# Performance work log

Measured on AMD Instinct MI355X. Metric: run time of the kernel, lower is better.

The kernel has to match this reference:

```python
import jax, jax.numpy as jnp
import numpy as np

THRESHOLD_PERCENTILE = 0.8  # init arg
B, H, W, C, N = 4, 256, 256, 128, 32


def _label_components(mask):
    """8-connected components via iterative min-label propagation.
    Background pixels get sentinel label BIG (== scipy label 0)."""
    h, w = mask.shape
    big = h * w
    init = jnp.where(mask, jnp.arange(big, dtype=jnp.int32).reshape(h, w), jnp.int32(big))

    def propagate(lbl):
        p = jnp.pad(lbl, 1, constant_values=big)
        # min over the 3x3 (8-connected incl. self) neighborhood
        nb = jnp.min(jnp.stack([p[di:di + h, dj:dj + w]
                                for di in range(3) for dj in range(3)]), axis=0)
        return jnp.where(mask, nb, jnp.int32(big))

    def cond(state):
        return ~state[1]

    def body(state):
        lbl, _ = state
        new = propagate(lbl)
        return new, jnp.all(new == lbl)

    lbl, _ = jax.lax.while_loop(cond, body, (init, jnp.array(False)))
    return lbl, jnp.int32(big)


def _merged_pairs_one(feat, centers):
    """feat: [H,W,C] float; centers: [N,2] int32. Returns merged-pair count."""
    h, w, c = feat.shape
    gt = feat[centers[:, 0], centers[:, 1]]                    # [N,C]
    flat = feat.reshape(-1, c)                                 # [HW,C]
    # euclidean cdist via norms (torch.cdist p=2)
    d2 = (jnp.sum(flat * flat, axis=1)[:, None]
          + jnp.sum(gt * gt, axis=1)[None, :]
          - 2.0 * flat @ gt.T)                                 # [HW,N]
    dists = jnp.sqrt(jnp.maximum(d2, 0.0))
    contrast = dists.min(axis=1).reshape(h, w)                 # [H,W]
    thr = jnp.percentile(contrast, THRESHOLD_PERCENTILE * 100.0)
    mask = contrast >= thr
    lbl, big = _label_components(mask)
    ids = lbl[centers[:, 0], centers[:, 1]]                    # [N]
    valid = ids != big                                         # scipy label > 0
    eq = (ids[:, None] == ids[None, :]) & valid[:, None]
    n = centers.shape[0]
    triu = jnp.triu(jnp.ones((n, n), dtype=bool), 1)           # i < j pairs
    return jnp.sum(eq & triu)


def setup_inputs() -> dict:
    key = jax.random.key(0)
    k1, k2 = jax.random.split(key)
    features = jax.random.normal(k1, (B, H, W, C), dtype=jnp.float32)
    gt_centers = jax.random.randint(k2, (B, N, 2), 0, H, dtype=jnp.int64)
    return {"features": features, "gt_centers": gt_centers}


def reference(features, gt_centers):
    centers = gt_centers.astype(jnp.int32)
    merged = jax.vmap(_merged_pairs_one)(features, centers)    # [B]
    n = centers.shape[1]
    total_pairs = features.shape[0] * (n * (n - 1) // 2)
    merge_rate = merged.sum().astype(jnp.float32) / jnp.float32(total_pairs)
    return merge_rate
```

## Files before the change

kernel.cpp:

```cpp
#include <hip/hip_runtime.h>
#include <stdint.h>

#define BB 4
#define HH 256
#define WW 256
#define CC 128
#define NN 32
#define NPIX (HH*WW)
#define RANK 52428u
#define TOTAL_PAIRS 1984.0f
#define CAND_MAX 8192u

#define OFF_KEYS 0
#define OFF_P    (BB*NPIX*4)
#define OFF_HIST (OFF_P + BB*NPIX*4)
#define OFF_THR  (OFF_HIST + BB*1024*4)
#define ZERO_BYTES (BB*1024*4)

typedef __attribute__((ext_vector_type(8))) short short8;
typedef __attribute__((ext_vector_type(4))) float f32x4;

__device__ __forceinline__ void split3(float f, short &hi, short &mid, short &lo) {
    uint32_t u  = __float_as_uint(f);
    uint32_t hb = u & 0xffff0000u;
    hi = (short)(hb >> 16);
    float r1 = f - __uint_as_float(hb);
    uint32_t mb = __float_as_uint(r1) & 0xffff0000u;
    mid = (short)(mb >> 16);
    float r2 = r1 - __uint_as_float(mb);
    lo = (short)(__float_as_uint(r2) >> 16);
}

__device__ __forceinline__ uint32_t qbin_of(uint32_t keybits) {
    float f = __uint_as_float(keybits);
    return (uint32_t)fminf(f * 128.0f, 65535.0f);
}

__global__ __launch_bounds__(256) void k_d2mfma(const float* __restrict__ feat,
        const int* __restrict__ centers, uint32_t* __restrict__ keys,
        uint32_t* __restrict__ hist) {
    __shared__ short gB[12288];
    __shared__ float gpart[32][8];
    __shared__ float gnormL[32];
    __shared__ uint32_t lhist[1024];
    int b = blockIdx.y;
    int tid = threadIdx.x;

    #pragma unroll
    for (int j = 0; j < 4; j++) lhist[tid + j*256] = 0u;

    {
        int n = tid & 31, j0 = tid >> 5;
        int cy = centers[(b*NN + n)*2 + 0];
        int cx = centers[(b*NN + n)*2 + 1];
        const float* gp = feat + ((size_t)(b << 16) + cy*WW + cx)*CC + j0*16;
        int tt = n >> 4, lane16 = n & 15, kk = j0 >> 1, qbase = (j0 & 1)*2;
        float ss = 0.f;
        #pragma unroll
        for (int hh = 0; hh < 2; hh++) {
            short8 vhi, vmid, vlo;
            #pragma unroll
            for (int u = 0; u < 8; u++) {
                float f = gp[hh*8 + u];
                ss = fmaf(f, f, ss);
                short a, bm, c; split3(f, a, bm, c);
                vhi[u] = a; vmid[u] = bm; vlo[u] = c;
            }
            int lane = (qbase + hh)*16 + lane16;
            int off = (tt*4 + kk)*512 + lane*8;
            *(short8*)&gB[off]        = vhi;
            *(short8*)&gB[off + 4096] = vmid;
            *(short8*)&gB[off + 8192] = vlo;
        }
        gpart[n][j0] = ss;
    }
    __syncthreads();
    if (tid < 32) {
        float s = 0.f;
        #pragma unroll
        for (int j = 0; j < 8; j++) s += gpart[tid][j];
        gnormL[tid] = s;
    }
    __syncthreads();

    int wv = tid >> 6, L = tid & 63;
    int m = L & 15, q = L >> 4;
    float gn0 = gnormL[m];
    float gn1 = gnormL[16 + m];

    for (int it = 0; it < 4; it++) {
        int p0 = blockIdx.x*256 + (wv*4 + it)*16;
        const float* fp = feat + ((size_t)(b << 16) + p0 + m)*CC + q*8;

        f32x4 acc[2] = {{0.f,0.f,0.f,0.f},{0.f,0.f,0.f,0.f}};
        float fn = 0.f;

        #pragma unroll
        for (int kk = 0; kk < 4; kk++) {
            float4 fa = *(const float4*)(fp + kk*32);
            float4 fb = *(const float4*)(fp + kk*32 + 4);
            float fs[8] = {fa.x,fa.y,fa.z,fa.w,fb.x,fb.y,fb.z,fb.w};
            short8 ahi, amid, alo;
            #pragma unroll
            for (int j = 0; j < 8; j++) {
                float f = fs[j];
                fn = fmaf(f, f, fn);
                short hh, md, lw; split3(f, hh, md, lw);
                ahi[j] = hh; amid[j] = md; alo[j] = lw;
            }
            #pragma unroll
            for (int t = 0; t < 2; t++) {
                int off = (t*4 + kk)*512 + L*8;
                short8 bhi = *(const short8*)&gB[off];
                short8 bmd = *(const short8*)&gB[off + 4096];
                short8 blo = *(const short8*)&gB[off + 8192];
                acc[t] = __builtin_amdgcn_mfma_f32_16x16x32_bf16(ahi,  bhi, acc[t], 0,0,0);
                acc[t] = __builtin_amdgcn_mfma_f32_16x16x32_bf16(ahi,  bmd, acc[t], 0,0,0);
                acc[t] = __builtin_amdgcn_mfma_f32_16x16x32_bf16(amid, bhi, acc[t], 0,0,0);
                acc[t] = __builtin_amdgcn_mfma_f32_16x16x32_bf16(ahi,  blo, acc[t], 0,0,0);
                acc[t] = __builtin_amdgcn_mfma_f32_16x16x32_bf16(amid, bmd, acc[t], 0,0,0);
                acc[t] = __builtin_amdgcn_mfma_f32_16x16x32_bf16(alo,  bhi, acc[t], 0,0,0);
            }
        }

        fn += __shfl_xor(fn, 16);
        fn += __shfl_xor(fn, 32);

        float vmin[4];
        #pragma unroll
        for (int r = 0; r < 4; r++) {
            float fnr = __shfl(fn, q*4 + r);
            float d0 = fnr + gn0 - 2.f*acc[0][r];
            float d1 = fnr + gn1 - 2.f*acc[1][r];
            float v = fminf(d0, d1);
            v = fminf(v, __shfl_xor(v, 1));
            v = fminf(v, __shfl_xor(v, 2));
            v = fminf(v, __shfl_xor(v, 4));
            v = fminf(v, __shfl_xor(v, 8));
            vmin[r] = v;
        }
        if (m < 4) {
            float v = (m==0) ? vmin[0] : (m==1) ? vmin[1] : (m==2) ? vmin[2] : vmin[3];
            if (!(v > 0.f)) v = 0.f;
            uint32_t kb = __float_as_uint(v);
            keys[(size_t)(b << 16) + p0 + q*4 + m] = kb;
            atomicAdd(&lhist[qbin_of(kb) >> 6], 1u);
        }
    }

    __syncthreads();
    #pragma unroll
    for (int j = 0; j < 4; j++) {
        int bin = tid + j*256;
        uint32_t hv = lhist[bin];
        if (hv) atomicAdd(&hist[(b << 10) + bin], hv);
    }
}

__global__ __launch_bounds__(1024) void k_selthr(const uint32_t* __restrict__ keys,
        const uint32_t* __restrict__ hist, uint32_t* __restrict__ thr_sm) {
    int b = blockIdx.x, t = threadIdx.x;
    __shared__ uint32_t wsum[16];
    __shared__ uint32_t sT1, sR1, sT, sR2, scnt, scnt2;
    __shared__ uint32_t fh[64];
    __shared__ uint32_t cand[CAND_MAX];
    __shared__ uint32_t cand2[2048];

    if (t < 64) fh[t] = 0;
    if (t == 0) { scnt = 0; scnt2 = 0; }

    int lane = t & 63, w = t >> 6;
    uint32_t s = hist[(b << 10) + t];
    uint32_t inc = s;
    #pragma unroll
    for (int off = 1; off < 64; off <<= 1) {
        uint32_t nb = __shfl_up((int)inc, off);
        if (lane >= off) inc += nb;
    }
    if (lane == 63) wsum[w] = inc;
    __syncthreads();
    if (t < 16) {
        uint32_t v = wsum[t];
        #pragma unroll
        for (int off = 1; off < 16; off <<= 1) {
            uint32_t nb = __shfl_up((int)v, off);
            if (t >= off) v += nb;
        }
        wsum[t] = v;
    }
    __syncthreads();
    uint32_t pre = ((w == 0) ? 0u : wsum[w-1]) + inc - s;
    if (pre <= RANK && RANK < pre + s) { sT1 = (uint32_t)t; sR1 = RANK - pre; }
    __syncthreads();
    uint32_t T1 = sT1, r1 = sR1;

    const uint4* kb = (const uint4*)(keys + ((size_t)b << 16));
    for (int i = t; i < NPIX/4; i += 1024) {
        uint4 k = kb[i];
        uint32_t q;
        #define PROC_KEY(X) { q = qbin_of(X); if ((q >> 6) == T1) { \
            atomicAdd(&fh[q & 63u], 1u); \
            uint32_t p = atomicAdd(&scnt, 1u); \
            if (p < CAND_MAX) cand[p] = (X); } }
        PROC_KEY(k.x) PROC_KEY(k.y) PROC_KEY(k.z) PROC_KEY(k.w)
        #undef PROC_KEY
    }
    __syncthreads();

    if (t < 64) {
        uint32_t s2 = fh[t];
        uint32_t inc2 = s2;
        #pragma unroll
        for (int off = 1; off < 64; off <<= 1) {
            uint32_t nb = __shfl_up((int)inc2, off);
            if (t >= off) inc2 += nb;
        }
        uint32_t pre2 = inc2 - s2;
        if (pre2 <= r1 && r1 < pre2 + s2) { sT = (T1 << 6) | (uint32_t)t; sR2 = r1 - pre2; }
    }
    __syncthreads();
    uint32_t T = sT, r2 = sR2;
    uint32_t K = scnt; if (K > CAND_MAX) K = CAND_MAX;

    for (uint32_t i = t; i < K; i += 1024) {
        uint32_t v = cand[i];
        if (qbin_of(v) == T) { uint32_t p = atomicAdd(&scnt2, 1u); if (p < 2048u) cand2[p] = v; }
    }
    __syncthreads();
    uint32_t K2 = scnt2; if (K2 > 2048u) K2 = 2048u;

    for (uint32_t i = t; i < K2; i += 1024) {
        uint32_t v = cand2[i];
        uint32_t less = 0, eq = 0;
        for (uint32_t j = 0; j < K2; j++) { uint32_t x = cand2[j]; less += (x < v); eq += (x == v); }
        if (less <= r2 && r2 < less + eq) thr_sm[b] = v;
    }
}

__global__ __launch_bounds__(256) void k_initrun(const uint32_t* __restrict__ keys,
        const uint32_t* __restrict__ thr_sm, int* __restrict__ P) {
    int b = blockIdx.y;
    int row = blockIdx.x, x = threadIdx.x;
    int p = row*256 + x;
    uint32_t thr = thr_sm[b];
    bool msk = keys[(b << 16) + p] >= thr;

    __shared__ int wmax[4];
    int lane = x & 63, w = x >> 6;
    int v = msk ? -1 : x;
    #pragma unroll
    for (int off = 1; off < 64; off <<= 1) {
        int nb = __shfl_up(v, off);
        if (lane >= off) v = max(v, nb);
    }
    if (lane == 63) wmax[w] = v;
    __syncthreads();
    int acc = v;
    for (int i = 0; i < w; i++) acc = max(acc, wmax[i]);
    P[(b << 16) + p] = msk ? (row*256 + acc + 1) : -1;
}

__device__ __forceinline__ int uf_find(int* P, int x) {
    while (true) {
        int p = P[x];
        if (p == x) return x;
        int gp = P[p];
        if (gp != p) P[x] = gp;
        x = gp;
    }
}
__device__ __forceinline__ void uf_unite(int* P, int a, int b) {
    while (true) {
        a = uf_find(P, a);
        b = uf_find(P, b);
        if (a == b) return;
        if (a > b) { int t = a; a = b; b = t; }
        int old = atomicCAS(&P[b], b, a);
        if (old == b) return;
        b = old;
    }
}
__global__ __launch_bounds__(256) void k_union(int* __restrict__ Pg) {
    int b = blockIdx.y;
    int p = blockIdx.x*256 + threadIdx.x;
    int* P = Pg + (b << 16);
    if (P[p] == -1) return;
    int y = p >> 8, x = p & 255;
    if (y == 0) return;
    bool ul = (x > 0)   && P[p-WW-1] != -1;
    bool uu =              P[p-WW]   != -1;
    bool ur = (x < 255) && P[p-WW+1] != -1;
    if (ul)        uf_unite(P, p, p-WW-1);
    if (uu && !ul) uf_unite(P, p, p-WW);
    if (ur && !uu) uf_unite(P, p, p-WW+1);
}

__global__ void k_pairs_fin(const int* __restrict__ centers, int* __restrict__ Pg,
                            float* __restrict__ out) {
    __shared__ int ids[BB*NN];
    __shared__ int total;
    int t = threadIdx.x;
    if (t == 0) total = 0;
    __syncthreads();
    if (t < BB*NN) {
        int b = t >> 5;
        int cy = centers[t*2 + 0];
        int cx = centers[t*2 + 1];
        int p = cy*WW + cx;
        const int* P = Pg + (b << 16);
        int id = P[p];
        if (id != -1) {
            int x = p;
            while (true) { int q = P[x]; if (q == x) break; x = q; }
            id = x;
        }
        ids[t] = id;
    }
    __syncthreads();
    int cnt = 0;
    if (t < BB*NN) {
        int b = t >> 5, n = t & 31;
        int id = ids[t];
        if (id != -1) for (int j = n+1; j < NN; j++) cnt += (ids[b*NN + j] == id);
    }
    if (cnt) atomicAdd(&total, cnt);
    __syncthreads();
    if (t == 0) out[0] = (float)total / TOTAL_PAIRS;
}

extern "C" void kernel_launch(void* const* d_in, const int* in_sizes, int n_in,
                              void* d_out, int out_size, void* d_ws, size_t ws_size,
                              hipStream_t stream) {
    const float* feat  = (const float*)d_in[0];
    const int* centers = (const int*)d_in[1];
    float* out         = (float*)d_out;
    char* ws           = (char*)d_ws;

    uint32_t* keys = (uint32_t*)(ws + OFF_KEYS);
    int*      Pg   = (int*)(ws + OFF_P);
    uint32_t* hist = (uint32_t*)(ws + OFF_HIST);
    uint32_t* thr  = (uint32_t*)(ws + OFF_THR);

    hipMemsetAsync(ws + OFF_HIST, 0, ZERO_BYTES, stream);

    dim3 gridPix(NPIX/256, BB);
    k_d2mfma    <<<gridPix, 256, 0, stream>>>(feat, centers, keys, hist);
    k_selthr    <<<BB, 1024, 0, stream>>>(keys, hist, thr);
    k_initrun   <<<gridPix, 256, 0, stream>>>(keys, thr, Pg);
    k_union     <<<gridPix, 256, 0, stream>>>(Pg);
    k_pairs_fin <<<1, 256, 0, stream>>>(centers, Pg, out);
}
```

Before: 232.8 us.

## Fuse CCL init, union and pair counting into one kernel with last-block finish

Merges the row-run init, union-find and pair-count kernels into a single kernel. Each block recomputes row-start labels for its own row and the row above in shared memory, unites only the run representatives, and the last block to finish (tracked by an atomic counter) counts the merged pairs. Parent storage becomes a zero-means-root encoding, so the memset initialises the union-find array instead of a separate write pass. This removes two kernel launches and a full label-array write pass, at the cost of a larger memset, duplicated scan work per block and a threadfence-based completion protocol.

```diff
diff --git a/kernel.cpp b/kernel.cpp
--- a/kernel.cpp
+++ b/kernel.cpp
@@ -11,11 +11,12 @@
 #define TOTAL_PAIRS 1984.0f
 #define CAND_MAX 8192u
 
-#define OFF_KEYS 0
-#define OFF_P    (BB*NPIX*4)
-#define OFF_HIST (OFF_P + BB*NPIX*4)
-#define OFF_THR  (OFF_HIST + BB*1024*4)
-#define ZERO_BYTES (BB*1024*4)
+#define OFF_HIST 0
+#define OFF_DONE (BB*1024*4)
+#define OFF_P    (OFF_DONE + 64)
+#define ZERO_BYTES (OFF_P + BB*NPIX*4)
+#define OFF_THR  ZERO_BYTES
+#define OFF_KEYS (OFF_THR + 64)
 
 typedef __attribute__((ext_vector_type(8))) short short8;
 typedef __attribute__((ext_vector_type(4))) float f32x4;
@@ -237,36 +238,15 @@
     }
 }
 
-__global__ __launch_bounds__(256) void k_initrun(const uint32_t* __restrict__ keys,
-        const uint32_t* __restrict__ thr_sm, int* __restrict__ P) {
-    int b = blockIdx.y;
-    int row = blockIdx.x, x = threadIdx.x;
-    int p = row*256 + x;
-    uint32_t thr = thr_sm[b];
-    bool msk = keys[(b << 16) + p] >= thr;
-
-    __shared__ int wmax[4];
-    int lane = x & 63, w = x >> 6;
-    int v = msk ? -1 : x;
-    #pragma unroll
-    for (int off = 1; off < 64; off <<= 1) {
-        int nb = __shfl_up(v, off);
-        if (lane >= off) v = max(v, nb);
-    }
-    if (lane == 63) wmax[w] = v;
-    __syncthreads();
-    int acc = v;
-    for (int i = 0; i < w; i++) acc = max(acc, wmax[i]);
-    P[(b << 16) + p] = msk ? (row*256 + acc + 1) : -1;
-}
-
 __device__ __forceinline__ int uf_find(int* P, int x) {
     while (true) {
-        int p = P[x];
-        if (p == x) return x;
-        int gp = P[p];
-        if (gp != p) P[x] = gp;
-        x = gp;
+        int v = P[x];
+        if (v == 0) return x;
+        int p = v - 1;
+        int gv = P[p];
+        if (gv == 0) return p;
+        P[x] = gv;
+        x = gv - 1;
     }
 }
 __device__ __forceinline__ void uf_unite(int* P, int a, int b) {
@@ -275,57 +255,103 @@
         b = uf_find(P, b);
         if (a == b) return;
         if (a > b) { int t = a; a = b; b = t; }
-        int old = atomicCAS(&P[b], b, a);
-        if (old == b) return;
-        b = old;
-    }
-}
-__global__ __launch_bounds__(256) void k_union(int* __restrict__ Pg) {
-    int b = blockIdx.y;
-    int p = blockIdx.x*256 + threadIdx.x;
+        int old = atomicCAS(&P[b], 0, a + 1);
+        if (old == 0) return;
+        b = old - 1;
+    }
+}
+
+__global__ __launch_bounds__(256) void k_ccl(const uint32_t* __restrict__ keys,
+        const uint32_t* __restrict__ thr_sm, const int* __restrict__ centers,
+        int* __restrict__ Pg, uint32_t* __restrict__ done, float* __restrict__ out) {
+    int bid = blockIdx.x;
+    int b = bid >> 8, rr = bid & 255;
+    int x = threadIdx.x;
+    __shared__ int up_rs[256];
+    __shared__ int swtmp[4];
+    __shared__ int ids[BB*NN];
+    __shared__ int stotal;
+    __shared__ bool isLast;
+
+    uint32_t thrv = thr_sm[b];
     int* P = Pg + (b << 16);
-    if (P[p] == -1) return;
-    int y = p >> 8, x = p & 255;
-    if (y == 0) return;
-    bool ul = (x > 0)   && P[p-WW-1] != -1;
-    bool uu =              P[p-WW]   != -1;
-    bool ur = (x < 255) && P[p-WW+1] != -1;
-    if (ul)        uf_unite(P, p, p-WW-1);
-    if (uu && !ul) uf_unite(P, p, p-WW);
-    if (ur && !uu) uf_unite(P, p, p-WW+1);
-}
-
-__global__ void k_pairs_fin(const int* __restrict__ centers, int* __restrict__ Pg,
-                            float* __restrict__ out) {
-    __shared__ int ids[BB*NN];
-    __shared__ int total;
-    int t = threadIdx.x;
-    if (t == 0) total = 0;
-    __syncthreads();
-    if (t < BB*NN) {
-        int b = t >> 5;
-        int cy = centers[t*2 + 0];
-        int cx = centers[t*2 + 1];
-        int p = cy*WW + cx;
-        const int* P = Pg + (b << 16);
-        int id = P[p];
-        if (id != -1) {
-            int x = p;
-            while (true) { int q = P[x]; if (q == x) break; x = q; }
-            id = x;
-        }
-        ids[t] = id;
+    int p = (rr << 8) + x;
+    bool msk = keys[((size_t)b << 16) + p] >= thrv;
+    int lane = x & 63, w = x >> 6;
+
+    int v = msk ? -1 : x;
+    #pragma unroll
+    for (int off = 1; off < 64; off <<= 1) {
+        int nb = __shfl_up(v, off);
+        if (lane >= off) v = max(v, nb);
+    }
+    if (lane == 63) swtmp[w] = v;
+    __syncthreads();
+    int acc = v;
+    for (int i = 0; i < w; i++) acc = max(acc, swtmp[i]);
+    int rs = (rr << 8) + acc + 1;
+    __syncthreads();
+
+    if (rr > 0) {
+        bool msku = keys[((size_t)b << 16) + p - WW] >= thrv;
+        int vu = msku ? -1 : x;
+        #pragma unroll
+        for (int off = 1; off < 64; off <<= 1) {
+            int nb = __shfl_up(vu, off);
+            if (lane >= off) vu = max(vu, nb);
+        }
+        if (lane == 63) swtmp[w] = vu;
+        __syncthreads();
+        int accu = vu;
+        for (int i = 0; i < w; i++) accu = max(accu, swtmp[i]);
+        up_rs[x] = msku ? (((rr - 1) << 8) + accu + 1) : -1;
+    }
+
+    if (msk && rs != p) P[p] = rs + 1;
+    __syncthreads();
+
+    if (rr > 0 && msk) {
+        bool ul = (x > 0)   && up_rs[x-1] >= 0;
+        bool uu =              up_rs[x]   >= 0;
+        bool ur = (x < 255) && up_rs[x+1] >= 0;
+        if (ul)        uf_unite(P, rs, up_rs[x-1]);
+        if (uu && !ul) uf_unite(P, rs, up_rs[x]);
+        if (ur && !uu) uf_unite(P, rs, up_rs[x+1]);
+    }
+
+    __threadfence();
+    __syncthreads();
+    if (x == 0) { uint32_t d = atomicAdd(done, 1u); isLast = (d == 1023u); }
+    __syncthreads();
+    if (!isLast) return;
+    __threadfence();
+
+    if (x == 0) stotal = 0;
+    __syncthreads();
+    if (x < BB*NN) {
+        int bb = x >> 5;
+        int cy = centers[x*2 + 0];
+        int cx = centers[x*2 + 1];
+        int pp = cy*WW + cx;
+        const int* Pb = Pg + (bb << 16);
+        int id = -1;
+        if (keys[((size_t)bb << 16) + pp] >= thr_sm[bb]) {
+            int xx = pp;
+            while (true) { int vv = Pb[xx]; if (vv == 0) break; xx = vv - 1; }
+            id = xx;
+        }
+        ids[x] = id;
     }
     __syncthreads();
     int cnt = 0;
-    if (t < BB*NN) {
-        int b = t >> 5, n = t & 31;
-        int id = ids[t];
-        if (id != -1) for (int j = n+1; j < NN; j++) cnt += (ids[b*NN + j] == id);
-    }
-    if (cnt) atomicAdd(&total, cnt);
-    __syncthreads();
-    if (t == 0) out[0] = (float)total / TOTAL_PAIRS;
+    if (x < BB*NN) {
+        int bb = x >> 5, n = x & 31;
+        int id = ids[x];
+        if (id != -1) for (int j = n + 1; j < NN; j++) cnt += (ids[bb*NN + j] == id);
+    }
+    if (cnt) atomicAdd(&stotal, cnt);
+    __syncthreads();
+    if (x == 0) out[0] = (float)stotal / TOTAL_PAIRS;
 }
 
 extern "C" void kernel_launch(void* const* d_in, const int* in_sizes, int n_in,
@@ -336,17 +362,16 @@
     float* out         = (float*)d_out;
     char* ws           = (char*)d_ws;
 
+    uint32_t* hist = (uint32_t*)(ws + OFF_HIST);
+    uint32_t* done = (uint32_t*)(ws + OFF_DONE);
+    int*      Pg   = (int*)(ws + OFF_P);
+    uint32_t* thr  = (uint32_t*)(ws + OFF_THR);
     uint32_t* keys = (uint32_t*)(ws + OFF_KEYS);
-    int*      Pg   = (int*)(ws + OFF_P);
-    uint32_t* hist = (uint32_t*)(ws + OFF_HIST);
-    uint32_t* thr  = (uint32_t*)(ws + OFF_THR);
-
-    hipMemsetAsync(ws + OFF_HIST, 0, ZERO_BYTES, stream);
+
+    hipMemsetAsync(ws, 0, ZERO_BYTES, stream);
 
     dim3 gridPix(NPIX/256, BB);
-    k_d2mfma    <<<gridPix, 256, 0, stream>>>(feat, centers, keys, hist);
-    k_selthr    <<<BB, 1024, 0, stream>>>(keys, hist, thr);
-    k_initrun   <<<gridPix, 256, 0, stream>>>(keys, thr, Pg);
-    k_union     <<<gridPix, 256, 0, stream>>>(Pg);
-    k_pairs_fin <<<1, 256, 0, stream>>>(centers, Pg, out);
-}
+    k_d2mfma <<<gridPix, 256, 0, stream>>>(feat, centers, keys, hist);
+    k_selthr <<<BB, 1024, 0, stream>>>(keys, hist, thr);
+    k_ccl    <<<HH*BB, 256, 0, stream>>>(keys, thr, centers, Pg, done, out);
+}
```

Result: slower. 295.4 us (+26.9%).
